# Optimization experiments

Measured on AMD Instinct MI355X. Metric: run time of the kernel, lower is better.

Reference implementation:

```python
import jax, jax.numpy as jnp
import numpy as np

CROSS_PRUNE = 0.1  # matches init_kwargs cross_prune

N, T, D, M = 100000, 64, 128, 8


def setup_inputs() -> dict:
    key = jax.random.key(0)
    k1, k2, k3, k4 = jax.random.split(key, 4)
    x = jax.random.normal(k1, (N, D), dtype=jnp.float32)          # graph node features
    mats = jax.random.normal(k2, (M, T, D), dtype=jnp.float32) * 0.1  # cross mats (kaiming-ish scale)
    head_w = jax.random.normal(k3, (M,), dtype=jnp.float32) * 0.3     # task_head.weight [1, M] squeezed
    head_b = jax.random.normal(k4, (), dtype=jnp.float32) * 0.1       # task_head.bias
    return {"x": x, "mats": mats, "head_w": head_w, "head_b": head_b}


def reference(x, mats, head_w, head_b):
    # Original: for each mat m, cross_dot_m = mat_m @ x.T  -> M mats of [T, N];
    # then per-(i,j): task_head([cross_dot_m[i,j] for m]) = sum_m w_m * cross_dot_m[i,j] + b.
    # Linearity lets us contract the head weight into the mats first (identical math,
    # avoids materializing the [M, T, N] stack the torch code builds element-by-element).
    w_mat = jnp.einsum('m,mtd->td', head_w, mats)          # [T, D]
    cross_dot = jnp.einsum('td,nd->tn', w_mat, x) + head_b  # [T, N]
    cross_sim = jax.nn.sigmoid(cross_dot)
    # prune: entries below threshold -> 0 (dense adjacency; edge_index extraction in the
    # original is just nonzero() over this matrix, which has data-dependent shape)
    cross_adj = jnp.where(cross_sim < CROSS_PRUNE, jnp.zeros_like(cross_sim), cross_sim)
    return cross_adj
```

## Files before the change

kernel.cpp:

```cpp
#include <hip/hip_runtime.h>
#include <hip/hip_bf16.h>

#define N_NODES 100000
#define T_DIM 64
#define D_DIM 128
#define M_MATS 8
#define CROSS_PRUNE 0.1f
#define WPLANE (T_DIM * D_DIM)

typedef __attribute__((ext_vector_type(8))) short bf16x8;
typedef __attribute__((ext_vector_type(4))) float f32x4;
typedef __attribute__((ext_vector_type(8))) unsigned short ushort8;

__device__ __forceinline__ void split3(float v, unsigned short& h,
                                       unsigned short& m, unsigned short& l) {
    __hip_bfloat16 bh = __float2bfloat16(v);
    float fh = __bfloat162float(bh);
    float r1 = v - fh;
    __hip_bfloat16 bm = __float2bfloat16(r1);
    float fm = __bfloat162float(bm);
    float r2 = r1 - fm;
    __hip_bfloat16 bl = __float2bfloat16(r2);
    h = __builtin_bit_cast(unsigned short, bh);
    m = __builtin_bit_cast(unsigned short, bm);
    l = __builtin_bit_cast(unsigned short, bl);
}

__global__ __launch_bounds__(256) void wsplit_kernel(const float* __restrict__ mats,
                                                     const float* __restrict__ head_w,
                                                     unsigned short* __restrict__ wh,
                                                     unsigned short* __restrict__ wm,
                                                     unsigned short* __restrict__ wl) {
    int i = blockIdx.x * 256 + threadIdx.x;
    if (i < WPLANE) {
        float acc = 0.f;
#pragma unroll
        for (int m = 0; m < M_MATS; ++m)
            acc += head_w[m] * mats[m * WPLANE + i];
        unsigned short h, mm, l;
        split3(acc, h, mm, l);
        wh[i] = h; wm[i] = mm; wl[i] = l;
    }
}

__global__ __launch_bounds__(256, 5) void cross_kernel(const float* __restrict__ x,
                                                       const unsigned short* __restrict__ wh,
                                                       const unsigned short* __restrict__ wm,
                                                       const unsigned short* __restrict__ wl,
                                                       const float* __restrict__ head_b_p,
                                                       float* __restrict__ out) {
    __shared__ unsigned short xh[64 * 64];
    __shared__ unsigned short xm[64 * 64];
    __shared__ unsigned short xl[64 * 64];

    const int tid = threadIdx.x;
    const int n0 = blockIdx.x * 64;
    const int lane = tid & 63;
    const int tg = tid >> 6;
    const int r = lane & 15;
    const int q = lane >> 4;

    const int srow = tid >> 2;
    const int scol = (tid & 3) * 16;
    const int gn_s = n0 + srow;
    const float* xrow = x + (size_t)gn_s * D_DIM + scol;

    float4 p0[4], p1[4];
#pragma unroll
    for (int j = 0; j < 4; ++j) {
        p0[j] = make_float4(0.f, 0.f, 0.f, 0.f);
        p1[j] = p0[j];
        if (gn_s < N_NODES) {
            p0[j] = *reinterpret_cast<const float4*>(xrow + j * 4);
            p1[j] = *reinterpret_cast<const float4*>(xrow + 64 + j * 4);
        }
    }

#define SPLIT_STORE16(P)                                                        \
    {                                                                           \
        float fv[16];                                                           \
        _Pragma("unroll")                                                       \
        for (int j = 0; j < 4; ++j) {                                           \
            fv[j * 4 + 0] = (P)[j].x; fv[j * 4 + 1] = (P)[j].y;                 \
            fv[j * 4 + 2] = (P)[j].z; fv[j * 4 + 3] = (P)[j].w;                 \
        }                                                                       \
        _Pragma("unroll")                                                       \
        for (int u = 0; u < 2; ++u) {                                           \
            ushort8 H, M, L;                                                    \
            _Pragma("unroll")                                                   \
            for (int e = 0; e < 8; ++e) {                                       \
                unsigned short h_, m_, l_;                                      \
                split3(fv[u * 8 + e], h_, m_, l_);                              \
                H[e] = h_; M[e] = m_; L[e] = l_;                                \
            }                                                                   \
            int unit = srow * 8 + (tid & 3) * 2 + u;                            \
            int byte = (unit << 4) ^ ((srow & 7) << 4);                         \
            *reinterpret_cast<ushort8*>(reinterpret_cast<char*>(xh) + byte) = H;\
            *reinterpret_cast<ushort8*>(reinterpret_cast<char*>(xm) + byte) = M;\
            *reinterpret_cast<ushort8*>(reinterpret_cast<char*>(xl) + byte) = L;\
        }                                                                       \
    }

    SPLIT_STORE16(p0);
    __syncthreads();

    f32x4 acc[4];
#pragma unroll
    for (int nt = 0; nt < 4; ++nt) acc[nt] = (f32x4){0.f, 0.f, 0.f, 0.f};

#pragma unroll
    for (int half = 0; half < 2; ++half) {
        if (half == 1) {
            __syncthreads();
            SPLIT_STORE16(p1);
            __syncthreads();
        }

        bf16x8 ah[2], am[2], al[2];
#pragma unroll
        for (int k4 = 0; k4 < 2; ++k4) {
            int eo = (tg * 16 + r) * D_DIM + half * 64 + k4 * 32 + q * 8;
            ah[k4] = *reinterpret_cast<const bf16x8*>(wh + eo);
            am[k4] = *reinterpret_cast<const bf16x8*>(wm + eo);
            al[k4] = *reinterpret_cast<const bf16x8*>(wl + eo);
        }

#pragma unroll
        for (int k4 = 0; k4 < 2; ++k4) {
#pragma unroll
            for (int np = 0; np < 4; np += 2) {
                bf16x8 bh0, bm0, bl0, bh1, bm1, bl1;
                {
                    int e0 = ((np * 16 + r) * 64 + k4 * 32 + q * 8);
                    int b0 = (e0 << 1) ^ ((r & 7) << 4);
                    int e1 = (((np + 1) * 16 + r) * 64 + k4 * 32 + q * 8);
                    int b1 = (e1 << 1) ^ ((r & 7) << 4);
                    bh0 = *reinterpret_cast<const bf16x8*>(reinterpret_cast<const char*>(xh) + b0);
                    bm0 = *reinterpret_cast<const bf16x8*>(reinterpret_cast<const char*>(xm) + b0);
                    bl0 = *reinterpret_cast<const bf16x8*>(reinterpret_cast<const char*>(xl) + b0);
                    bh1 = *reinterpret_cast<const bf16x8*>(reinterpret_cast<const char*>(xh) + b1);
                    bm1 = *reinterpret_cast<const bf16x8*>(reinterpret_cast<const char*>(xm) + b1);
                    bl1 = *reinterpret_cast<const bf16x8*>(reinterpret_cast<const char*>(xl) + b1);
                }
                acc[np]     = __builtin_amdgcn_mfma_f32_16x16x32_bf16(ah[k4], bh0, acc[np], 0, 0, 0);
                acc[np + 1] = __builtin_amdgcn_mfma_f32_16x16x32_bf16(ah[k4], bh1, acc[np + 1], 0, 0, 0);
                acc[np]     = __builtin_amdgcn_mfma_f32_16x16x32_bf16(ah[k4], bm0, acc[np], 0, 0, 0);
                acc[np + 1] = __builtin_amdgcn_mfma_f32_16x16x32_bf16(ah[k4], bm1, acc[np + 1], 0, 0, 0);
                acc[np]     = __builtin_amdgcn_mfma_f32_16x16x32_bf16(am[k4], bh0, acc[np], 0, 0, 0);
                acc[np + 1] = __builtin_amdgcn_mfma_f32_16x16x32_bf16(am[k4], bh1, acc[np + 1], 0, 0, 0);
                acc[np]     = __builtin_amdgcn_mfma_f32_16x16x32_bf16(ah[k4], bl0, acc[np], 0, 0, 0);
                acc[np + 1] = __builtin_amdgcn_mfma_f32_16x16x32_bf16(ah[k4], bl1, acc[np + 1], 0, 0, 0);
                acc[np]     = __builtin_amdgcn_mfma_f32_16x16x32_bf16(al[k4], bh0, acc[np], 0, 0, 0);
                acc[np + 1] = __builtin_amdgcn_mfma_f32_16x16x32_bf16(al[k4], bh1, acc[np + 1], 0, 0, 0);
                acc[np]     = __builtin_amdgcn_mfma_f32_16x16x32_bf16(am[k4], bm0, acc[np], 0, 0, 0);
                acc[np + 1] = __builtin_amdgcn_mfma_f32_16x16x32_bf16(am[k4], bm1, acc[np + 1], 0, 0, 0);
            }
        }
    }

    const float hb = head_b_p[0];
#pragma unroll
    for (int nt = 0; nt < 4; ++nt) {
        int n = n0 + nt * 16 + r;
        if (n < N_NODES) {
#pragma unroll
            for (int i = 0; i < 4; ++i) {
                int t = tg * 16 + q * 4 + i;
                float v = acc[nt][i] + hb;
                float s = 1.0f / (1.0f + __expf(-v));
                if (s < CROSS_PRUNE) s = 0.0f;
                out[(size_t)t * N_NODES + n] = s;
            }
        }
    }
#undef SPLIT_STORE16
}

extern "C" void kernel_launch(void* const* d_in, const int* in_sizes, int n_in,
                              void* d_out, int out_size, void* d_ws, size_t ws_size,
                              hipStream_t stream) {
    const float* x      = (const float*)d_in[0];
    const float* mats   = (const float*)d_in[1];
    const float* head_w = (const float*)d_in[2];
    const float* head_b = (const float*)d_in[3];
    float* out = (float*)d_out;

    unsigned short* wh = (unsigned short*)d_ws;
    unsigned short* wm = wh + WPLANE;
    unsigned short* wl = wm + WPLANE;

    hipLaunchKernelGGL(wsplit_kernel, dim3((WPLANE + 255) / 256), dim3(256), 0, stream,
                       mats, head_w, wh, wm, wl);

    int nblk = (N_NODES + 63) / 64;
    hipLaunchKernelGGL(cross_kernel, dim3(nblk), dim3(256), 0, stream,
                       x, wh, wm, wl, head_b, out);
}
```

Measured before the change: 33.00 us.

## Fuse weight contraction into persistent cross kernel with prefetched node chunks

Removes the separate weight-split kernel: each block now contracts head_w into mats and splits the result into bf16 hi/mid/lo fragments directly in registers, once per block. The grid becomes 521 persistent blocks that each process 3 chunks of 64 nodes, with the full 128-wide x tile staged in shared memory and the next chunk's x loaded into registers while the current chunk computes. This cuts a kernel launch and the workspace round trip. In exchange, every block redundantly reads all 8 mats planes, shared memory use grows to 48KB per block, and occupancy drops (launch bounds 256,2).

Result: slower. 57.24 us (+73.4%).

```diff
diff --git a/kernel.cpp b/kernel.cpp
--- a/kernel.cpp
+++ b/kernel.cpp
@@ -6,7 +6,9 @@
 #define D_DIM 128
 #define M_MATS 8
 #define CROSS_PRUNE 0.1f
-#define WPLANE (T_DIM * D_DIM)
+#define NCHUNK 1563
+#define GRID 521
+#define CPB 3
 
 typedef __attribute__((ext_vector_type(8))) short bf16x8;
 typedef __attribute__((ext_vector_type(4))) float f32x4;
@@ -26,66 +28,74 @@
     l = __builtin_bit_cast(unsigned short, bl);
 }
 
-__global__ __launch_bounds__(256) void wsplit_kernel(const float* __restrict__ mats,
-                                                     const float* __restrict__ head_w,
-                                                     unsigned short* __restrict__ wh,
-                                                     unsigned short* __restrict__ wm,
-                                                     unsigned short* __restrict__ wl) {
-    int i = blockIdx.x * 256 + threadIdx.x;
-    if (i < WPLANE) {
-        float acc = 0.f;
-#pragma unroll
-        for (int m = 0; m < M_MATS; ++m)
-            acc += head_w[m] * mats[m * WPLANE + i];
-        unsigned short h, mm, l;
-        split3(acc, h, mm, l);
-        wh[i] = h; wm[i] = mm; wl[i] = l;
-    }
-}
-
-__global__ __launch_bounds__(256, 5) void cross_kernel(const float* __restrict__ x,
-                                                       const unsigned short* __restrict__ wh,
-                                                       const unsigned short* __restrict__ wm,
-                                                       const unsigned short* __restrict__ wl,
+__global__ __launch_bounds__(256, 2) void fused_kernel(const float* __restrict__ x,
+                                                       const float* __restrict__ mats,
+                                                       const float* __restrict__ head_w,
                                                        const float* __restrict__ head_b_p,
                                                        float* __restrict__ out) {
-    __shared__ unsigned short xh[64 * 64];
-    __shared__ unsigned short xm[64 * 64];
-    __shared__ unsigned short xl[64 * 64];
+    __shared__ unsigned short xh[T_DIM * D_DIM / 2 * 2];
+    __shared__ unsigned short xm[8192];
+    __shared__ unsigned short xl[8192];
 
     const int tid = threadIdx.x;
-    const int n0 = blockIdx.x * 64;
     const int lane = tid & 63;
     const int tg = tid >> 6;
     const int r = lane & 15;
     const int q = lane >> 4;
-
     const int srow = tid >> 2;
-    const int scol = (tid & 3) * 16;
-    const int gn_s = n0 + srow;
-    const float* xrow = x + (size_t)gn_s * D_DIM + scol;
-
-    float4 p0[4], p1[4];
-#pragma unroll
-    for (int j = 0; j < 4; ++j) {
-        p0[j] = make_float4(0.f, 0.f, 0.f, 0.f);
-        p1[j] = p0[j];
-        if (gn_s < N_NODES) {
-            p0[j] = *reinterpret_cast<const float4*>(xrow + j * 4);
-            p1[j] = *reinterpret_cast<const float4*>(xrow + 64 + j * 4);
-        }
-    }
-
-#define SPLIT_STORE16(P)                                                        \
+    const int c4 = tid & 3;
+
+    int n0 = blockIdx.x * 64;
+    float4 p[8];
+    {
+        const int gn = n0 + srow;
+        const float* xrow = x + (size_t)gn * D_DIM + c4 * 32;
+#pragma unroll
+        for (int j = 0; j < 8; ++j) {
+            p[j] = make_float4(0.f, 0.f, 0.f, 0.f);
+            if (gn < N_NODES) p[j] = *reinterpret_cast<const float4*>(xrow + j * 4);
+        }
+    }
+
+    float hw[M_MATS];
+#pragma unroll
+    for (int m = 0; m < M_MATS; ++m) hw[m] = head_w[m];
+
+    bf16x8 ah[4], am[4], al[4];
+#pragma unroll
+    for (int k4 = 0; k4 < 4; ++k4) {
+        const float* wp = mats + (tg * 16 + r) * D_DIM + k4 * 32 + q * 8;
+        float wa[8];
+#pragma unroll
+        for (int e = 0; e < 8; ++e) wa[e] = 0.f;
+#pragma unroll
+        for (int m = 0; m < M_MATS; ++m) {
+            float4 v0 = *reinterpret_cast<const float4*>(wp + m * (T_DIM * D_DIM));
+            float4 v1 = *reinterpret_cast<const float4*>(wp + m * (T_DIM * D_DIM) + 4);
+            wa[0] = fmaf(hw[m], v0.x, wa[0]); wa[1] = fmaf(hw[m], v0.y, wa[1]);
+            wa[2] = fmaf(hw[m], v0.z, wa[2]); wa[3] = fmaf(hw[m], v0.w, wa[3]);
+            wa[4] = fmaf(hw[m], v1.x, wa[4]); wa[5] = fmaf(hw[m], v1.y, wa[5]);
+            wa[6] = fmaf(hw[m], v1.z, wa[6]); wa[7] = fmaf(hw[m], v1.w, wa[7]);
+        }
+#pragma unroll
+        for (int e = 0; e < 8; ++e) {
+            unsigned short h_, m_, l_;
+            split3(wa[e], h_, m_, l_);
+            ah[k4][e] = (short)h_; am[k4][e] = (short)m_; al[k4][e] = (short)l_;
+        }
+    }
+    const float hb = head_b_p[0];
+
+#define SPLIT_STORE32(P)                                                        \
     {                                                                           \
-        float fv[16];                                                           \
+        float fv[32];                                                           \
         _Pragma("unroll")                                                       \
-        for (int j = 0; j < 4; ++j) {                                           \
+        for (int j = 0; j < 8; ++j) {                                           \
             fv[j * 4 + 0] = (P)[j].x; fv[j * 4 + 1] = (P)[j].y;                 \
             fv[j * 4 + 2] = (P)[j].z; fv[j * 4 + 3] = (P)[j].w;                 \
         }                                                                       \
         _Pragma("unroll")                                                       \
-        for (int u = 0; u < 2; ++u) {                                           \
+        for (int u = 0; u < 4; ++u) {                                           \
             ushort8 H, M, L;                                                    \
             _Pragma("unroll")                                                   \
             for (int e = 0; e < 8; ++e) {                                       \
@@ -93,7 +103,7 @@
                 split3(fv[u * 8 + e], h_, m_, l_);                              \
                 H[e] = h_; M[e] = m_; L[e] = l_;                                \
             }                                                                   \
-            int unit = srow * 8 + (tid & 3) * 2 + u;                            \
+            int unit = srow * 16 + c4 * 4 + u;                                  \
             int byte = (unit << 4) ^ ((srow & 7) << 4);                         \
             *reinterpret_cast<ushort8*>(reinterpret_cast<char*>(xh) + byte) = H;\
             *reinterpret_cast<ushort8*>(reinterpret_cast<char*>(xm) + byte) = M;\
@@ -101,47 +111,42 @@
         }                                                                       \
     }
 
-    SPLIT_STORE16(p0);
+    SPLIT_STORE32(p);
     __syncthreads();
 
-    f32x4 acc[4];
-#pragma unroll
-    for (int nt = 0; nt < 4; ++nt) acc[nt] = (f32x4){0.f, 0.f, 0.f, 0.f};
-
-#pragma unroll
-    for (int half = 0; half < 2; ++half) {
-        if (half == 1) {
-            __syncthreads();
-            SPLIT_STORE16(p1);
-            __syncthreads();
-        }
-
-        bf16x8 ah[2], am[2], al[2];
-#pragma unroll
-        for (int k4 = 0; k4 < 2; ++k4) {
-            int eo = (tg * 16 + r) * D_DIM + half * 64 + k4 * 32 + q * 8;
-            ah[k4] = *reinterpret_cast<const bf16x8*>(wh + eo);
-            am[k4] = *reinterpret_cast<const bf16x8*>(wm + eo);
-            al[k4] = *reinterpret_cast<const bf16x8*>(wl + eo);
-        }
-
-#pragma unroll
-        for (int k4 = 0; k4 < 2; ++k4) {
+#pragma unroll
+    for (int c = 0; c < CPB; ++c) {
+        n0 = (c * GRID + (int)blockIdx.x) * 64;
+
+        float4 pn[8];
+        if (c + 1 < CPB) {
+            const int gn = ((c + 1) * GRID + (int)blockIdx.x) * 64 + srow;
+            const float* xrow = x + (size_t)gn * D_DIM + c4 * 32;
+#pragma unroll
+            for (int j = 0; j < 8; ++j) {
+                pn[j] = make_float4(0.f, 0.f, 0.f, 0.f);
+                if (gn < N_NODES) pn[j] = *reinterpret_cast<const float4*>(xrow + j * 4);
+            }
+        }
+
+        f32x4 acc[4];
+#pragma unroll
+        for (int nt = 0; nt < 4; ++nt) acc[nt] = (f32x4){0.f, 0.f, 0.f, 0.f};
+
+#pragma unroll
+        for (int k4 = 0; k4 < 4; ++k4) {
 #pragma unroll
             for (int np = 0; np < 4; np += 2) {
-                bf16x8 bh0, bm0, bl0, bh1, bm1, bl1;
-                {
-                    int e0 = ((np * 16 + r) * 64 + k4 * 32 + q * 8);
-                    int b0 = (e0 << 1) ^ ((r & 7) << 4);
-                    int e1 = (((np + 1) * 16 + r) * 64 + k4 * 32 + q * 8);
-                    int b1 = (e1 << 1) ^ ((r & 7) << 4);
-                    bh0 = *reinterpret_cast<const bf16x8*>(reinterpret_cast<const char*>(xh) + b0);
-                    bm0 = *reinterpret_cast<const bf16x8*>(reinterpret_cast<const char*>(xm) + b0);
-                    bl0 = *reinterpret_cast<const bf16x8*>(reinterpret_cast<const char*>(xl) + b0);
-                    bh1 = *reinterpret_cast<const bf16x8*>(reinterpret_cast<const char*>(xh) + b1);
-                    bm1 = *reinterpret_cast<const bf16x8*>(reinterpret_cast<const char*>(xm) + b1);
-                    bl1 = *reinterpret_cast<const bf16x8*>(reinterpret_cast<const char*>(xl) + b1);
-                }
+                int e0 = ((np * 16 + r) * D_DIM + k4 * 32 + q * 8);
+                int b0 = (e0 << 1) ^ ((r & 7) << 4);
+                int e1 = (((np + 1) * 16 + r) * D_DIM + k4 * 32 + q * 8);
+                int b1 = (e1 << 1) ^ ((r & 7) << 4);
+                bf16x8 bh0 = *reinterpret_cast<const bf16x8*>(reinterpret_cast<const char*>(xh) + b0);
+                bf16x8 bm0 = *reinterpret_cast<const bf16x8*>(reinterpret_cast<const char*>(xm) + b0);
+                bf16x8 bl0 = *reinterpret_cast<const bf16x8*>(reinterpret_cast<const char*>(xl) + b0);
+                bf16x8 bh1 = *reinterpret_cast<const bf16x8*>(reinterpret_cast<const char*>(xh) + b1);
+                bf16x8 bm1 = *reinterpret_cast<const bf16x8*>(reinterpret_cast<const char*>(xm) + b1);
+                bf16x8 bl1 = *reinterpret_cast<const bf16x8*>(reinterpret_cast<const char*>(xl) + b1);
                 acc[np]     = __builtin_amdgcn_mfma_f32_16x16x32_bf16(ah[k4], bh0, acc[np], 0, 0, 0);
                 acc[np + 1] = __builtin_amdgcn_mfma_f32_16x16x32_bf16(ah[k4], bh1, acc[np + 1], 0, 0, 0);
                 acc[np]     = __builtin_amdgcn_mfma_f32_16x16x32_bf16(ah[k4], bm0, acc[np], 0, 0, 0);
@@ -156,24 +161,29 @@
                 acc[np + 1] = __builtin_amdgcn_mfma_f32_16x16x32_bf16(am[k4], bm1, acc[np + 1], 0, 0, 0);
             }
         }
-    }
-
-    const float hb = head_b_p[0];
-#pragma unroll
-    for (int nt = 0; nt < 4; ++nt) {
-        int n = n0 + nt * 16 + r;
-        if (n < N_NODES) {
-#pragma unroll
-            for (int i = 0; i < 4; ++i) {
-                int t = tg * 16 + q * 4 + i;
-                float v = acc[nt][i] + hb;
-                float s = 1.0f / (1.0f + __expf(-v));
-                if (s < CROSS_PRUNE) s = 0.0f;
-                out[(size_t)t * N_NODES + n] = s;
+
+#pragma unroll
+        for (int nt = 0; nt < 4; ++nt) {
+            int n = n0 + nt * 16 + r;
+            if (n < N_NODES) {
+#pragma unroll
+                for (int i = 0; i < 4; ++i) {
+                    int t = tg * 16 + q * 4 + i;
+                    float v = acc[nt][i] + hb;
+                    float s = 1.0f / (1.0f + __expf(-v));
+                    if (s < CROSS_PRUNE) s = 0.0f;
+                    out[(size_t)t * N_NODES + n] = s;
+                }
             }
         }
-    }
-#undef SPLIT_STORE16
+
+        if (c + 1 < CPB) {
+            __syncthreads();
+            SPLIT_STORE32(pn);
+            __syncthreads();
+        }
+    }
+#undef SPLIT_STORE32
 }
 
 extern "C" void kernel_launch(void* const* d_in, const int* in_sizes, int n_in,
@@ -185,14 +195,6 @@
     const float* head_b = (const float*)d_in[3];
     float* out = (float*)d_out;
 
-    unsigned short* wh = (unsigned short*)d_ws;
-    unsigned short* wm = wh + WPLANE;
-    unsigned short* wl = wm + WPLANE;
-
-    hipLaunchKernelGGL(wsplit_kernel, dim3((WPLANE + 255) / 256), dim3(256), 0, stream,
-                       mats, head_w, wh, wm, wl);
-
-    int nblk = (N_NODES + 63) / 64;
-    hipLaunchKernelGGL(cross_kernel, dim3(nblk), dim3(256), 0, stream,
-                       x, wh, wm, wl, head_b, out);
+    hipLaunchKernelGGL(fused_kernel, dim3(GRID), dim3(256), 0, stream,
+                       x, mats, head_w, head_b, out);
 }
```

## Process two 64-node chunks per block and prefetch the next chunk's x during compute

Applied to the files above, without the earlier changes.

The cross kernel now launches a fixed grid of 782 blocks, and each block handles two 64-node chunks strided by the grid size. While the second half of the current chunk's MFMA work runs, the block loads the next chunk's x rows into registers, overlapping global loads with compute. The change halves the block count, which amortizes the per-block launch and setup cost. In exchange it raises register pressure (occupancy hint lowered from 5 to 4 waves), adds extra barriers, and with only 782 blocks the tail may balance less evenly across CUs.

Measured after the change: 36.37 us. 1.1x slower.

```diff
diff --git a/kernel.cpp b/kernel.cpp
--- a/kernel.cpp
+++ b/kernel.cpp
@@ -7,6 +7,8 @@
 #define M_MATS 8
 #define CROSS_PRUNE 0.1f
 #define WPLANE (T_DIM * D_DIM)
+#define GRID 782
+#define CPB 2
 
 typedef __attribute__((ext_vector_type(8))) short bf16x8;
 typedef __attribute__((ext_vector_type(4))) float f32x4;
@@ -43,7 +45,7 @@
     }
 }
 
-__global__ __launch_bounds__(256, 5) void cross_kernel(const float* __restrict__ x,
+__global__ __launch_bounds__(256, 4) void cross_kernel(const float* __restrict__ x,
                                                        const unsigned short* __restrict__ wh,
                                                        const unsigned short* __restrict__ wm,
                                                        const unsigned short* __restrict__ wl,
@@ -54,25 +56,26 @@
     __shared__ unsigned short xl[64 * 64];
 
     const int tid = threadIdx.x;
-    const int n0 = blockIdx.x * 64;
     const int lane = tid & 63;
     const int tg = tid >> 6;
     const int r = lane & 15;
     const int q = lane >> 4;
-
     const int srow = tid >> 2;
     const int scol = (tid & 3) * 16;
-    const int gn_s = n0 + srow;
-    const float* xrow = x + (size_t)gn_s * D_DIM + scol;
+    const float hb = head_b_p[0];
 
     float4 p0[4], p1[4];
-#pragma unroll
-    for (int j = 0; j < 4; ++j) {
-        p0[j] = make_float4(0.f, 0.f, 0.f, 0.f);
-        p1[j] = p0[j];
-        if (gn_s < N_NODES) {
-            p0[j] = *reinterpret_cast<const float4*>(xrow + j * 4);
-            p1[j] = *reinterpret_cast<const float4*>(xrow + 64 + j * 4);
+    {
+        const int gn = blockIdx.x * 64 + srow;
+        const float* xrow = x + (size_t)gn * D_DIM + scol;
+#pragma unroll
+        for (int j = 0; j < 4; ++j) {
+            p0[j] = make_float4(0.f, 0.f, 0.f, 0.f);
+            p1[j] = p0[j];
+            if (gn < N_NODES) {
+                p0[j] = *reinterpret_cast<const float4*>(xrow + j * 4);
+                p1[j] = *reinterpret_cast<const float4*>(xrow + 64 + j * 4);
+            }
         }
     }
 
@@ -101,77 +104,130 @@
         }                                                                       \
     }
 
-    SPLIT_STORE16(p0);
-    __syncthreads();
-
-    f32x4 acc[4];
-#pragma unroll
-    for (int nt = 0; nt < 4; ++nt) acc[nt] = (f32x4){0.f, 0.f, 0.f, 0.f};
-
-#pragma unroll
-    for (int half = 0; half < 2; ++half) {
-        if (half == 1) {
-            __syncthreads();
-            SPLIT_STORE16(p1);
-            __syncthreads();
-        }
-
-        bf16x8 ah[2], am[2], al[2];
-#pragma unroll
-        for (int k4 = 0; k4 < 2; ++k4) {
-            int eo = (tg * 16 + r) * D_DIM + half * 64 + k4 * 32 + q * 8;
-            ah[k4] = *reinterpret_cast<const bf16x8*>(wh + eo);
-            am[k4] = *reinterpret_cast<const bf16x8*>(wm + eo);
-            al[k4] = *reinterpret_cast<const bf16x8*>(wl + eo);
-        }
-
-#pragma unroll
-        for (int k4 = 0; k4 < 2; ++k4) {
-#pragma unroll
-            for (int np = 0; np < 4; np += 2) {
-                bf16x8 bh0, bm0, bl0, bh1, bm1, bl1;
-                {
+#pragma unroll
+    for (int c = 0; c < CPB; ++c) {
+        const int n0 = (c * GRID + (int)blockIdx.x) * 64;
+
+        SPLIT_STORE16(p0);
+        __syncthreads();
+
+        f32x4 acc[4];
+#pragma unroll
+        for (int nt = 0; nt < 4; ++nt) acc[nt] = (f32x4){0.f, 0.f, 0.f, 0.f};
+
+        {
+            bf16x8 ah[2], am[2], al[2];
+#pragma unroll
+            for (int k4 = 0; k4 < 2; ++k4) {
+                int eo = (tg * 16 + r) * D_DIM + k4 * 32 + q * 8;
+                ah[k4] = *reinterpret_cast<const bf16x8*>(wh + eo);
+                am[k4] = *reinterpret_cast<const bf16x8*>(wm + eo);
+                al[k4] = *reinterpret_cast<const bf16x8*>(wl + eo);
+            }
+#pragma unroll
+            for (int k4 = 0; k4 < 2; ++k4) {
+#pragma unroll
+                for (int np = 0; np < 4; np += 2) {
                     int e0 = ((np * 16 + r) * 64 + k4 * 32 + q * 8);
                     int b0 = (e0 << 1) ^ ((r & 7) << 4);
                     int e1 = (((np + 1) * 16 + r) * 64 + k4 * 32 + q * 8);
                     int b1 = (e1 << 1) ^ ((r & 7) << 4);
-                    bh0 = *reinterpret_cast<const bf16x8*>(reinterpret_cast<const char*>(xh) + b0);
-                    bm0 = *reinterpret_cast<const bf16x8*>(reinterpret_cast<const char*>(xm) + b0);
-                    bl0 = *reinterpret_cast<const bf16x8*>(reinterpret_cast<const char*>(xl) + b0);
-                    bh1 = *reinterpret_cast<const bf16x8*>(reinterpret_cast<const char*>(xh) + b1);
-                    bm1 = *reinterpret_cast<const bf16x8*>(reinterpret_cast<const char*>(xm) + b1);
-                    bl1 = *reinterpret_cast<const bf16x8*>(reinterpret_cast<const char*>(xl) + b1);
-                }
-                acc[np]     = __builtin_amdgcn_mfma_f32_16x16x32_bf16(ah[k4], bh0, acc[np], 0, 0, 0);
-                acc[np + 1] = __builtin_amdgcn_mfma_f32_16x16x32_bf16(ah[k4], bh1, acc[np + 1], 0, 0, 0);
-                acc[np]     = __builtin_amdgcn_mfma_f32_16x16x32_bf16(ah[k4], bm0, acc[np], 0, 0, 0);
-                acc[np + 1] = __builtin_amdgcn_mfma_f32_16x16x32_bf16(ah[k4], bm1, acc[np + 1], 0, 0, 0);
-                acc[np]     = __builtin_amdgcn_mfma_f32_16x16x32_bf16(am[k4], bh0, acc[np], 0, 0, 0);
-                acc[np + 1] = __builtin_amdgcn_mfma_f32_16x16x32_bf16(am[k4], bh1, acc[np + 1], 0, 0, 0);
-                acc[np]     = __builtin_amdgcn_mfma_f32_16x16x32_bf16(ah[k4], bl0, acc[np], 0, 0, 0);
-                acc[np + 1] = __builtin_amdgcn_mfma_f32_16x16x32_bf16(ah[k4], bl1, acc[np + 1], 0, 0, 0);
-                acc[np]     = __builtin_amdgcn_mfma_f32_16x16x32_bf16(al[k4], bh0, acc[np], 0, 0, 0);
-                acc[np + 1] = __builtin_amdgcn_mfma_f32_16x16x32_bf16(al[k4], bh1, acc[np + 1], 0, 0, 0);
-                acc[np]     = __builtin_amdgcn_mfma_f32_16x16x32_bf16(am[k4], bm0, acc[np], 0, 0, 0);
-                acc[np + 1] = __builtin_amdgcn_mfma_f32_16x16x32_bf16(am[k4], bm1, acc[np + 1], 0, 0, 0);
-            }
-        }
-    }
-
-    const float hb = head_b_p[0];
-#pragma unroll
-    for (int nt = 0; nt < 4; ++nt) {
-        int n = n0 + nt * 16 + r;
-        if (n < N_NODES) {
-#pragma unroll
-            for (int i = 0; i < 4; ++i) {
-                int t = tg * 16 + q * 4 + i;
-                float v = acc[nt][i] + hb;
-                float s = 1.0f / (1.0f + __expf(-v));
-                if (s < CROSS_PRUNE) s = 0.0f;
-                out[(size_t)t * N_NODES + n] = s;
-            }
-        }
+                    bf16x8 bh0 = *reinterpret_cast<const bf16x8*>(reinterpret_cast<const char*>(xh) + b0);
+                    bf16x8 bm0 = *reinterpret_cast<const bf16x8*>(reinterpret_cast<const char*>(xm) + b0);
+                    bf16x8 bl0 = *reinterpret_cast<const bf16x8*>(reinterpret_cast<const char*>(xl) + b0);
+                    bf16x8 bh1 = *reinterpret_cast<const bf16x8*>(reinterpret_cast<const char*>(xh) + b1);
+                    bf16x8 bm1 = *reinterpret_cast<const bf16x8*>(reinterpret_cast<const char*>(xm) + b1);
+                    bf16x8 bl1 = *reinterpret_cast<const bf16x8*>(reinterpret_cast<const char*>(xl) + b1);
+                    acc[np]     = __builtin_amdgcn_mfma_f32_16x16x32_bf16(ah[k4], bh0, acc[np], 0, 0, 0);
+                    acc[np + 1] = __builtin_amdgcn_mfma_f32_16x16x32_bf16(ah[k4], bh1, acc[np + 1], 0, 0, 0);
+                    acc[np]     = __builtin_amdgcn_mfma_f32_16x16x32_bf16(ah[k4], bm0, acc[np], 0, 0, 0);
+                    acc[np + 1] = __builtin_amdgcn_mfma_f32_16x16x32_bf16(ah[k4], bm1, acc[np + 1], 0, 0, 0);
+                    acc[np]     = __builtin_amdgcn_mfma_f32_16x16x32_bf16(am[k4], bh0, acc[np], 0, 0, 0);
+                    acc[np + 1] = __builtin_amdgcn_mfma_f32_16x16x32_bf16(am[k4], bh1, acc[np + 1], 0, 0, 0);
+                    acc[np]     = __builtin_amdgcn_mfma_f32_16x16x32_bf16(ah[k4], bl0, acc[np], 0, 0, 0);
+                    acc[np + 1] = __builtin_amdgcn_mfma_f32_16x16x32_bf16(ah[k4], bl1, acc[np + 1], 0, 0, 0);
+                    acc[np]     = __builtin_amdgcn_mfma_f32_16x16x32_bf16(al[k4], bh0, acc[np], 0, 0, 0);
+                    acc[np + 1] = __builtin_amdgcn_mfma_f32_16x16x32_bf16(al[k4], bh1, acc[np + 1], 0, 0, 0);
+                    acc[np]     = __builtin_amdgcn_mfma_f32_16x16x32_bf16(am[k4], bm0, acc[np], 0, 0, 0);
+                    acc[np + 1] = __builtin_amdgcn_mfma_f32_16x16x32_bf16(am[k4], bm1, acc[np + 1], 0, 0, 0);
+                }
+            }
+        }
+
+        __syncthreads();
+        SPLIT_STORE16(p1);
+        __syncthreads();
+
+        if (c + 1 < CPB) {
+            const int gn = ((c + 1) * GRID + (int)blockIdx.x) * 64 + srow;
+            const float* xrow = x + (size_t)gn * D_DIM + scol;
+#pragma unroll
+            for (int j = 0; j < 4; ++j) {
+                float4 a = make_float4(0.f, 0.f, 0.f, 0.f);
+                float4 b = a;
+                if (gn < N_NODES) {
+                    a = *reinterpret_cast<const float4*>(xrow + j * 4);
+                    b = *reinterpret_cast<const float4*>(xrow + 64 + j * 4);
+                }
+                p0[j] = a; p1[j] = b;
+            }
+        }
+
+        {
+            bf16x8 ah[2], am[2], al[2];
+#pragma unroll
+            for (int k4 = 0; k4 < 2; ++k4) {
+                int eo = (tg * 16 + r) * D_DIM + 64 + k4 * 32 + q * 8;
+                ah[k4] = *reinterpret_cast<const bf16x8*>(wh + eo);
+                am[k4] = *reinterpret_cast<const bf16x8*>(wm + eo);
+                al[k4] = *reinterpret_cast<const bf16x8*>(wl + eo);
+            }
+#pragma unroll
+            for (int k4 = 0; k4 < 2; ++k4) {
+#pragma unroll
+                for (int np = 0; np < 4; np += 2) {
+                    int e0 = ((np * 16 + r) * 64 + k4 * 32 + q * 8);
+                    int b0 = (e0 << 1) ^ ((r & 7) << 4);
+                    int e1 = (((np + 1) * 16 + r) * 64 + k4 * 32 + q * 8);
+                    int b1 = (e1 << 1) ^ ((r & 7) << 4);
+                    bf16x8 bh0 = *reinterpret_cast<const bf16x8*>(reinterpret_cast<const char*>(xh) + b0);
+                    bf16x8 bm0 = *reinterpret_cast<const bf16x8*>(reinterpret_cast<const char*>(xm) + b0);
+                    bf16x8 bl0 = *reinterpret_cast<const bf16x8*>(reinterpret_cast<const char*>(xl) + b0);
+                    bf16x8 bh1 = *reinterpret_cast<const bf16x8*>(reinterpret_cast<const char*>(xh) + b1);
+                    bf16x8 bm1 = *reinterpret_cast<const bf16x8*>(reinterpret_cast<const char*>(xm) + b1);
+                    bf16x8 bl1 = *reinterpret_cast<const bf16x8*>(reinterpret_cast<const char*>(xl) + b1);
+                    acc[np]     = __builtin_amdgcn_mfma_f32_16x16x32_bf16(ah[k4], bh0, acc[np], 0, 0, 0);
+                    acc[np + 1] = __builtin_amdgcn_mfma_f32_16x16x32_bf16(ah[k4], bh1, acc[np + 1], 0, 0, 0);
+                    acc[np]     = __builtin_amdgcn_mfma_f32_16x16x32_bf16(ah[k4], bm0, acc[np], 0, 0, 0);
+                    acc[np + 1] = __builtin_amdgcn_mfma_f32_16x16x32_bf16(ah[k4], bm1, acc[np + 1], 0, 0, 0);
+                    acc[np]     = __builtin_amdgcn_mfma_f32_16x16x32_bf16(am[k4], bh0, acc[np], 0, 0, 0);
+                    acc[np + 1] = __builtin_amdgcn_mfma_f32_16x16x32_bf16(am[k4], bh1, acc[np + 1], 0, 0, 0);
+                    acc[np]     = __builtin_amdgcn_mfma_f32_16x16x32_bf16(ah[k4], bl0, acc[np], 0, 0, 0);
+                    acc[np + 1] = __builtin_amdgcn_mfma_f32_16x16x32_bf16(ah[k4], bl1, acc[np + 1], 0, 0, 0);
+                    acc[np]     = __builtin_amdgcn_mfma_f32_16x16x32_bf16(al[k4], bh0, acc[np], 0, 0, 0);
+                    acc[np + 1] = __builtin_amdgcn_mfma_f32_16x16x32_bf16(al[k4], bh1, acc[np + 1], 0, 0, 0);
+                    acc[np]     = __builtin_amdgcn_mfma_f32_16x16x32_bf16(am[k4], bm0, acc[np], 0, 0, 0);
+                    acc[np + 1] = __builtin_amdgcn_mfma_f32_16x16x32_bf16(am[k4], bm1, acc[np + 1], 0, 0, 0);
+                }
+            }
+        }
+
+#pragma unroll
+        for (int nt = 0; nt < 4; ++nt) {
+            int n = n0 + nt * 16 + r;
+            if (n < N_NODES) {
+#pragma unroll
+                for (int i = 0; i < 4; ++i) {
+                    int t = tg * 16 + q * 4 + i;
+                    float v = acc[nt][i] + hb;
+                    float s = 1.0f / (1.0f + __expf(-v));
+                    if (s < CROSS_PRUNE) s = 0.0f;
+                    out[(size_t)t * N_NODES + n] = s;
+                }
+            }
+        }
+
+        if (c + 1 < CPB) __syncthreads();
     }
 #undef SPLIT_STORE16
 }
@@ -192,7 +248,6 @@
     hipLaunchKernelGGL(wsplit_kernel, dim3((WPLANE + 255) / 256), dim3(256), 0, stream,
                        mats, head_w, wh, wm, wl);
 
-    int nblk = (N_NODES + 63) / 64;
-    hipLaunchKernelGGL(cross_kernel, dim3(nblk), dim3(256), 0, stream,
+    hipLaunchKernelGGL(cross_kernel, dim3(GRID), dim3(256), 0, stream,
                        x, wh, wm, wl, head_b, out);
 }
```
